# Optimization experiments

Measured on AMD Instinct MI355X. Metric: run time of the kernel, lower is better.

The kernel has to match this reference:

```python
import jax, jax.numpy as jnp
import numpy as np

K = 1024          # number of knots (len(self.knots))
SAMPLES = 4096    # outSamples
S = SAMPLES - 1   # xIter has samples-1 points


def irregular_gauss(x, mean, low_std, high_std):
    # std = lowStd if x <= mean else highStd; std = exp(std)
    std = jnp.exp(jnp.where(x <= mean, low_std, high_std))
    return jnp.exp(-0.5 * jnp.square((x - mean) / std))


def setup_inputs() -> dict:
    key = jax.random.key(0)
    ks = jax.random.split(key, 8)
    x = jax.random.uniform(ks[0], (K,), dtype=jnp.float32)
    smear_window = jnp.array([0.125, 0.125], dtype=jnp.float32)  # (lowerSmear, upperSmear)
    knot_mean = 0.1 * jax.random.normal(ks[1], (K,), dtype=jnp.float32)
    knot_low = 0.1 * jax.random.normal(ks[2], (K,), dtype=jnp.float32)
    knot_high = 0.1 * jax.random.normal(ks[3], (K,), dtype=jnp.float32)
    ent_mean = 0.1 * jax.random.normal(ks[4], (K,), dtype=jnp.float32)
    ent_low = 0.1 * jax.random.normal(ks[5], (K,), dtype=jnp.float32)
    ent_high = 0.1 * jax.random.normal(ks[6], (K,), dtype=jnp.float32)
    polarization = 0.1 * jax.random.normal(ks[7], (K,), dtype=jnp.float32)
    return {"x": x, "smear_window": smear_window, "knot_mean": knot_mean,
            "knot_low": knot_low, "knot_high": knot_high, "ent_mean": ent_mean,
            "ent_low": ent_low, "ent_high": ent_high, "polarization": polarization}


def reference(x, smear_window, knot_mean, knot_low, knot_high,
              ent_mean, ent_low, ent_high, polarization):
    lower, upper = smear_window[0], smear_window[1]
    x_step = ((upper - lower) * x) / SAMPLES            # [K]
    x_low = (1.0 - lower) * x                           # [K]
    x_iter = jnp.arange(S, dtype=x.dtype) / SAMPLES     # [S]

    # per-knot smear curves: knot_k applied over its smeared window  -> [K, S]
    grid = x_step[:, None] * x_iter[None, :] + x_low[:, None]
    smear = irregular_gauss(grid, knot_mean[:, None], knot_low[:, None], knot_high[:, None])
    signal = jnp.fft.fft(smear, axis=-1)                # [K, S] complex

    # correlation_ij = mean_s ifft(sig_i * conj(sig_j))  ==  (sig_i[0]*conj(sig_j[0])) / S
    corr = (signal[:, None, 0] * jnp.conj(signal[None, :, 0])).real / S  # [K, K]
    # entangleActivation[j] (a LinearGuass) applied to correlation_ij
    mix = irregular_gauss(corr, ent_mean[None, :], ent_low[None, :], ent_high[None, :])
    mask = 1.0 - jnp.eye(K, dtype=x.dtype)              # skip idx == jdx
    mixm = mix * mask                                   # [K, K]

    # superposition = outer(sig_j, sig_i); row/col collapse then ifft.
    # By FFT linearity: ifft(sig_i * sum(sig_j)) = sum(sig_j) * smear_i, and symmetrically.
    sum_sig = jnp.sum(signal, axis=-1)                  # [K] complex; smears are real -> Re used
    cosp, sinp = jnp.cos(polarization), jnp.sin(polarization)

    coef1 = mixm @ (cosp * sum_sig.real)                                 # [K]
    term1 = coef1[:, None] * smear                                       # cos branch
    term2 = sum_sig.real[:, None] * jnp.einsum('ij,js->is', mixm * sinp[None, :], smear)  # sin branch
    term3 = jnp.sum(mask - mixm, axis=1)[:, None] * smear                # classical mix (1-mix)*smear
    result = jnp.sum(term1 + term2 + term3, axis=0)                      # [S]

    # trailing gaussian envelope, summed over knots
    lows = (1.0 - lower) * x
    highs = (1.0 + upper) * x
    g_samples = (highs - lows)[:, None] * x_iter[None, :] + lows[:, None]  # [K, S]
    gauss = irregular_gauss(g_samples, x[:, None], lows[:, None], highs[:, None])
    return jnp.sum(gauss, axis=0) * result              # [S]
```

## Files before the change

kernel.cpp:

```cpp
#include <hip/hip_runtime.h>
#include <math.h>

#define K 1024
#define SAMPLES 4096
#define S (SAMPLES - 1)

__device__ __forceinline__ float ig(float x, float mean, float lo, float hi) {
    float sel = (x <= mean) ? lo : hi;
    float z = (x - mean) * __expf(-sel);
    return __expf(-0.5f * z * z);
}

__device__ __forceinline__ float block_reduce256(float v, float* sm) {
    #pragma unroll
    for (int o = 32; o > 0; o >>= 1) v += __shfl_down(v, o, 64);
    int lane = threadIdx.x & 63, w = threadIdx.x >> 6;
    if (lane == 0) sm[w] = v;
    __syncthreads();
    float r = 0.f;
    if (threadIdx.x == 0) r = sm[0] + sm[1] + sm[2] + sm[3];
    __syncthreads();
    return r;
}

__global__ __launch_bounds__(256) void k_smear_sums(
    const float* __restrict__ x, const float* __restrict__ sw,
    const float* __restrict__ km, const float* __restrict__ kl, const float* __restrict__ kh,
    float* __restrict__ A, float* __restrict__ R)
{
    __shared__ float sm[4];
    int k = blockIdx.x;
    float lower = sw[0], upper = sw[1];
    float xk = x[k];
    float x_step = (upper - lower) * xk * (1.0f / SAMPLES);
    float x_low = (1.0f - lower) * xk;
    float mean = km[k], lo = kl[k], hi = kh[k];
    float sum = 0.f;
    for (int s = threadIdx.x; s < S; s += 256) {
        float g = x_step * ((float)s * (1.0f / SAMPLES)) + x_low;
        sum += ig(g, mean, lo, hi);
    }
    float tot = block_reduce256(sum, sm);
    if (threadIdx.x == 0) {
        A[k] = tot;
        R[k] = (float)S * ig(x_low, mean, lo, hi);
    }
}

__global__ __launch_bounds__(256) void k_entangle(
    const float* __restrict__ A, const float* __restrict__ R,
    const float* __restrict__ em, const float* __restrict__ el, const float* __restrict__ eh,
    const float* __restrict__ pol,
    float* __restrict__ coef1, float* __restrict__ colsum, float* __restrict__ M)
{
    __shared__ float sm0[4], sm1[4];
    int b = blockIdx.x;
    if (b < K) {
        int i = b;
        float Ai = A[i];
        float c = 0.f, m = 0.f;
        for (int j = threadIdx.x; j < K; j += 256) {
            if (j == i) continue;
            float corr = Ai * A[j] * (1.0f / S);
            float mix = ig(corr, em[j], el[j], eh[j]);
            c += mix * __cosf(pol[j]) * R[j];
            m += mix;
        }
        float ct = block_reduce256(c, sm0);
        float mt = block_reduce256(m, sm1);
        if (threadIdx.x == 0) { coef1[i] = ct; M[i] = mt; }
    } else {
        int j = b - K;
        float Aj = A[j];
        float mean = em[j], lo = el[j], hi = eh[j];
        float cs = 0.f;
        for (int i = threadIdx.x; i < K; i += 256) {
            if (i == j) continue;
            float corr = A[i] * Aj * (1.0f / S);
            cs += R[i] * ig(corr, mean, lo, hi);
        }
        float ct = block_reduce256(cs, sm0);
        if (threadIdx.x == 0) colsum[j] = ct;
    }
}

#define SB 16
#define NC 32
#define KPC (K / NC)
__global__ __launch_bounds__(256) void k_accumulate(
    const float* __restrict__ x, const float* __restrict__ sw,
    const float* __restrict__ km, const float* __restrict__ kl, const float* __restrict__ kh,
    const float* __restrict__ pol,
    const float* __restrict__ coef1, const float* __restrict__ colsum, const float* __restrict__ M,
    float* __restrict__ res, float* __restrict__ env)
{
    int sb = blockIdx.x % SB;
    int kc = blockIdx.x / SB;
    int s = sb * 256 + threadIdx.x;
    if (s >= S) return;
    float xi = (float)s * (1.0f / SAMPLES);
    float lower = sw[0], upper = sw[1];
    float rsum = 0.f, esum = 0.f;
    int k0 = kc * KPC;
    #pragma unroll 4
    for (int k = k0; k < k0 + KPC; ++k) {
        float xk = x[k];
        float x_step = (upper - lower) * xk * (1.0f / SAMPLES);
        float x_low = (1.0f - lower) * xk;
        float smear = ig(x_step * xi + x_low, km[k], kl[k], kh[k]);
        float w = coef1[k] + __sinf(pol[k]) * colsum[k] + (float)(K - 1) - M[k];
        rsum += w * smear;
        float lows = x_low;
        float highs = (1.0f + upper) * xk;
        float g = (highs - lows) * xi + lows;
        esum += ig(g, xk, lows, highs);
    }
    atomicAdd(&res[s], rsum);
    atomicAdd(&env[s], esum);
}

__global__ __launch_bounds__(256) void k_final(
    const float* __restrict__ res, const float* __restrict__ env, float* __restrict__ out)
{
    int s = blockIdx.x * 256 + threadIdx.x;
    if (s < S) out[s] = env[s] * res[s];
}

extern "C" void kernel_launch(void* const* d_in, const int* in_sizes, int n_in,
                              void* d_out, int out_size, void* d_ws, size_t ws_size,
                              hipStream_t stream)
{
    const float* x   = (const float*)d_in[0];
    const float* sw  = (const float*)d_in[1];
    const float* km  = (const float*)d_in[2];
    const float* kl  = (const float*)d_in[3];
    const float* kh  = (const float*)d_in[4];
    const float* em  = (const float*)d_in[5];
    const float* el  = (const float*)d_in[6];
    const float* eh  = (const float*)d_in[7];
    const float* pol = (const float*)d_in[8];
    float* out = (float*)d_out;

    float* A      = (float*)d_ws;
    float* R      = A + K;
    float* coef1  = R + K;
    float* colsum = coef1 + K;
    float* M      = colsum + K;
    float* res    = M + K;
    float* env    = res + S;

    hipMemsetAsync(res, 0, 2 * S * sizeof(float), stream);
    k_smear_sums<<<K, 256, 0, stream>>>(x, sw, km, kl, kh, A, R);
    k_entangle<<<2 * K, 256, 0, stream>>>(A, R, em, el, eh, pol, coef1, colsum, M);
    k_accumulate<<<SB * NC, 256, 0, stream>>>(x, sw, km, kl, kh, pol, coef1, colsum, M, res, env);
    k_final<<<16, 256, 0, stream>>>(res, env, out);
}
```

Baseline: 91.75 us.

## Fuse entangle row/column passes and replace atomic accumulation with warp-reduced output

```diff
diff --git a/kernel.cpp b/kernel.cpp
--- a/kernel.cpp
+++ b/kernel.cpp
@@ -47,83 +47,61 @@
     }
 }
 
-__global__ __launch_bounds__(256) void k_entangle(
+__global__ __launch_bounds__(256) void k_weights(
     const float* __restrict__ A, const float* __restrict__ R,
     const float* __restrict__ em, const float* __restrict__ el, const float* __restrict__ eh,
-    const float* __restrict__ pol,
-    float* __restrict__ coef1, float* __restrict__ colsum, float* __restrict__ M)
+    const float* __restrict__ pol, float* __restrict__ w)
 {
-    __shared__ float sm0[4], sm1[4];
-    int b = blockIdx.x;
-    if (b < K) {
-        int i = b;
-        float Ai = A[i];
-        float c = 0.f, m = 0.f;
-        for (int j = threadIdx.x; j < K; j += 256) {
-            if (j == i) continue;
-            float corr = Ai * A[j] * (1.0f / S);
-            float mix = ig(corr, em[j], el[j], eh[j]);
-            c += mix * __cosf(pol[j]) * R[j];
-            m += mix;
-        }
-        float ct = block_reduce256(c, sm0);
-        float mt = block_reduce256(m, sm1);
-        if (threadIdx.x == 0) { coef1[i] = ct; M[i] = mt; }
-    } else {
-        int j = b - K;
-        float Aj = A[j];
-        float mean = em[j], lo = el[j], hi = eh[j];
-        float cs = 0.f;
-        for (int i = threadIdx.x; i < K; i += 256) {
-            if (i == j) continue;
-            float corr = A[i] * Aj * (1.0f / S);
-            cs += R[i] * ig(corr, mean, lo, hi);
-        }
-        float ct = block_reduce256(cs, sm0);
-        if (threadIdx.x == 0) colsum[j] = ct;
+    __shared__ float sm0[4], sm1[4], sm2[4];
+    int t = blockIdx.x;
+    float At = A[t];
+    float emt = em[t], elt = el[t], eht = eh[t];
+    float c = 0.f, m = 0.f, cs = 0.f;
+    for (int u = threadIdx.x; u < K; u += 256) {
+        if (u == t) continue;
+        float corr = At * A[u] * (1.0f / S);
+        float mr = ig(corr, em[u], el[u], eh[u]);
+        float mc = ig(corr, emt, elt, eht);
+        float Ru = R[u];
+        c += mr * __cosf(pol[u]) * Ru;
+        m += mr;
+        cs += Ru * mc;
     }
+    float ct = block_reduce256(c, sm0);
+    float mt = block_reduce256(m, sm1);
+    float cst = block_reduce256(cs, sm2);
+    if (threadIdx.x == 0)
+        w[t] = ct + __sinf(pol[t]) * cst + (float)(K - 1) - mt;
 }
 
-#define SB 16
-#define NC 32
-#define KPC (K / NC)
-__global__ __launch_bounds__(256) void k_accumulate(
+__global__ __launch_bounds__(256) void k_output(
     const float* __restrict__ x, const float* __restrict__ sw,
     const float* __restrict__ km, const float* __restrict__ kl, const float* __restrict__ kh,
-    const float* __restrict__ pol,
-    const float* __restrict__ coef1, const float* __restrict__ colsum, const float* __restrict__ M,
-    float* __restrict__ res, float* __restrict__ env)
+    const float* __restrict__ w, float* __restrict__ out)
 {
-    int sb = blockIdx.x % SB;
-    int kc = blockIdx.x / SB;
-    int s = sb * 256 + threadIdx.x;
+    int t = blockIdx.x * 256 + threadIdx.x;
+    int s = t >> 4;
+    int sub = t & 15;
     if (s >= S) return;
     float xi = (float)s * (1.0f / SAMPLES);
     float lower = sw[0], upper = sw[1];
     float rsum = 0.f, esum = 0.f;
-    int k0 = kc * KPC;
-    #pragma unroll 4
-    for (int k = k0; k < k0 + KPC; ++k) {
+    for (int k = sub; k < K; k += 16) {
         float xk = x[k];
         float x_step = (upper - lower) * xk * (1.0f / SAMPLES);
         float x_low = (1.0f - lower) * xk;
         float smear = ig(x_step * xi + x_low, km[k], kl[k], kh[k]);
-        float w = coef1[k] + __sinf(pol[k]) * colsum[k] + (float)(K - 1) - M[k];
-        rsum += w * smear;
-        float lows = x_low;
+        rsum += w[k] * smear;
         float highs = (1.0f + upper) * xk;
-        float g = (highs - lows) * xi + lows;
-        esum += ig(g, xk, lows, highs);
+        float g = (highs - x_low) * xi + x_low;
+        esum += ig(g, xk, x_low, highs);
     }
-    atomicAdd(&res[s], rsum);
-    atomicAdd(&env[s], esum);
-}
-
-__global__ __launch_bounds__(256) void k_final(
-    const float* __restrict__ res, const float* __restrict__ env, float* __restrict__ out)
-{
-    int s = blockIdx.x * 256 + threadIdx.x;
-    if (s < S) out[s] = env[s] * res[s];
+    #pragma unroll
+    for (int o = 8; o > 0; o >>= 1) {
+        rsum += __shfl_down(rsum, o, 16);
+        esum += __shfl_down(esum, o, 16);
+    }
+    if (sub == 0) out[s] = rsum * esum;
 }
 
 extern "C" void kernel_launch(void* const* d_in, const int* in_sizes, int n_in,
@@ -141,17 +119,11 @@
     const float* pol = (const float*)d_in[8];
     float* out = (float*)d_out;
 
-    float* A      = (float*)d_ws;
-    float* R      = A + K;
-    float* coef1  = R + K;
-    float* colsum = coef1 + K;
-    float* M      = colsum + K;
-    float* res    = M + K;
-    float* env    = res + S;
+    float* A = (float*)d_ws;
+    float* R = A + K;
+    float* w = R + K;
 
-    hipMemsetAsync(res, 0, 2 * S * sizeof(float), stream);
     k_smear_sums<<<K, 256, 0, stream>>>(x, sw, km, kl, kh, A, R);
-    k_entangle<<<2 * K, 256, 0, stream>>>(A, R, em, el, eh, pol, coef1, colsum, M);
-    k_accumulate<<<SB * NC, 256, 0, stream>>>(x, sw, km, kl, kh, pol, coef1, colsum, M, res, env);
-    k_final<<<16, 256, 0, stream>>>(res, env, out);
+    k_weights<<<K, 256, 0, stream>>>(A, R, em, el, eh, pol, w);
+    k_output<<<(SAMPLES * 16) / 256, 256, 0, stream>>>(x, sw, km, kl, kh, w, out);
 }
```

After: 94.93 us. 3.5% more time.
